# Kernel optimization log

Measured on AMD Instinct MI355X. Metric: run time of the kernel, lower is better.

Reference implementation:

```python
import jax, jax.numpy as jnp
import numpy as np

N_BOTTLENECK = 256  # must be a power of two for the butterfly network


def butterfly_ortho(x, theta, first_output_entry_positive=False):
    """FFT-like butterfly of Givens rotations over the last dim (size n, power of 2).
    Stage s pairs indices (i, i + 2^s); each pair gets one rotation angle.
    theta has (n/2)*log2(n) entries, consumed stage by stage.
    """
    n = x.shape[-1]
    stages = int(np.log2(n))
    idx = 0
    for s in range(stages):
        stride = 1 << s
        nb = n // (2 * stride)
        th = theta[idx: idx + n // 2].reshape(nb, stride)
        idx += n // 2
        xr = x.reshape(-1, nb, 2, stride)  # [B, blocks, half, offset]
        a, b = xr[:, :, 0, :], xr[:, :, 1, :]
        c, sn = jnp.cos(th), jnp.sin(th)
        a2 = c * a - sn * b
        b2 = sn * a + c * b
        x = jnp.stack([a2, b2], axis=2).reshape(-1, n)
    if first_output_entry_positive:
        # convention flag: force sign of first output entry non-negative
        x = x.at[:, 0].set(jnp.abs(x[:, 0]))
    return x


def setup_inputs() -> dict:
    key = jax.random.key(0)
    ks = jax.random.split(key, 12)
    dims = [4096, 1024, 256, 1024, 4096]
    B = 16384

    def w(k, i, o):
        return (jax.random.normal(k, (i, o), dtype=jnp.float32) * (1.0 / np.sqrt(i)))

    inp = {
        "x": jax.random.normal(ks[0], (B, dims[0]), dtype=jnp.float32),
        "enc_w0": w(ks[1], dims[0], dims[1]),
        "enc_b0": jnp.zeros((dims[1],), jnp.float32),
        "enc_w1": w(ks[2], dims[1], dims[2]),
        "enc_b1": jnp.zeros((dims[2],), jnp.float32),
        "theta": jax.random.normal(ks[3], ((dims[2] // 2) * int(np.log2(dims[2])),), dtype=jnp.float32),
        "dec_w0": w(ks[4], dims[2], dims[3]),
        "dec_b0": jnp.zeros((dims[3],), jnp.float32),
        "out_w": w(ks[5], dims[3], dims[4]),
        "out_b": jnp.zeros((dims[4],), jnp.float32),
    }
    return inp


def reference(x, enc_w0, enc_b0, enc_w1, enc_b1, theta, dec_w0, dec_b0, out_w, out_b):
    # encoder: Linear + ReLU stack
    h = jax.nn.relu(x @ enc_w0 + enc_b0)
    h = jax.nn.relu(h @ enc_w1 + enc_b1)
    # orthogonal butterfly network at the bottleneck
    h = butterfly_ortho(h, theta, first_output_entry_positive=False)
    # decoder: Linear + ReLU stack, then plain Linear output layer
    h = jax.nn.relu(h @ dec_w0 + dec_b0)
    out = h @ out_w + out_b
    return out
```

## Files before the change

kernel.cpp:

```cpp
#include <hip/hip_runtime.h>

typedef __attribute__((ext_vector_type(8))) short short8v;
typedef __attribute__((ext_vector_type(4))) float f32x4;
typedef __attribute__((ext_vector_type(4))) unsigned int uint4v;
typedef __attribute__((ext_vector_type(4))) float float4v;

__device__ __forceinline__ unsigned short f2bf(float f) {
  union { float f; unsigned u; } v; v.f = f;
  unsigned r = v.u + 0x7fffu + ((v.u >> 16) & 1u);
  return (unsigned short)(r >> 16);
}
__device__ __forceinline__ float bf2f(unsigned short h) {
  union { unsigned u; float f; } v; v.u = ((unsigned)h) << 16;
  return v.f;
}
__device__ __forceinline__ unsigned pack2(float a, float b) {
  return (unsigned)f2bf(a) | ((unsigned)f2bf(b) << 16);
}

__device__ __forceinline__ void gload_lds16(const void* g, void* l) {
  __builtin_amdgcn_global_load_lds(
      (const __attribute__((address_space(1))) void*)g,
      (__attribute__((address_space(3))) void*)l, 16, 0, 0);
}

#define SBAR() __builtin_amdgcn_s_barrier()
#define SCHED0() __builtin_amdgcn_sched_barrier(0)
#define LGKM(n) do { asm volatile("s_waitcnt lgkmcnt(" #n ")" ::: "memory"); \
                     __builtin_amdgcn_sched_barrier(0); } while (0)
#define VMW(n) asm volatile("s_waitcnt vmcnt(" #n ")" ::: "memory")

__global__ void f32_to_bf16(const float* __restrict__ in, unsigned short* __restrict__ out,
                            size_t n8) {
  size_t i = (size_t)blockIdx.x * blockDim.x + threadIdx.x;
  const size_t stride = (size_t)gridDim.x * blockDim.x;
  for (; i < n8; i += stride) {
    const float4v* p = (const float4v*)(in + i * 8);
    float4v a = __builtin_nontemporal_load(p);
    float4v b = __builtin_nontemporal_load(p + 1);
    uint4v r;
    r.x = pack2(a.x, a.y); r.y = pack2(a.z, a.w);
    r.z = pack2(b.x, b.y); r.w = pack2(b.z, b.w);
    *(uint4v*)(out + i * 8) = r;
  }
}

__global__ void transpose_bf16(const float* __restrict__ W, unsigned short* __restrict__ WT,
                               int K, int N) {
  __shared__ float t[32][33];
  const int kb = blockIdx.x * 32, nb = blockIdx.y * 32;
  const int tx = threadIdx.x, ty = threadIdx.y;
  #pragma unroll
  for (int y = 0; y < 4; ++y)
    t[ty + y*8][tx] = W[(size_t)(kb + ty + y*8) * N + nb + tx];
  __syncthreads();
  #pragma unroll
  for (int y = 0; y < 4; ++y) {
    const int n = nb + ty + y*8;
    WT[(size_t)n * K + kb + tx] = f2bf(t[tx][ty + y*8]);
  }
}

__global__ void trig_kernel(const float* __restrict__ theta, float* __restrict__ ct,
                            float* __restrict__ st, int n) {
  const int i = blockIdx.x * 256 + threadIdx.x;
  if (i < n) {
    float s, c;
    sincosf(theta[i], &s, &c);
    ct[i] = c; st[i] = s;
  }
}

__global__ void butterfly_kernel(const unsigned short* __restrict__ X,
                                 unsigned short* __restrict__ Y,
                                 const float* __restrict__ ct, const float* __restrict__ st) {
  __shared__ float L[2][256];
  const int tid = threadIdx.x;
  const size_t base = (size_t)blockIdx.x * 512;
  const unsigned v = *(const unsigned*)(X + base + tid * 2);
  const int r = tid >> 7;
  const int col = (tid * 2) & 255;
  L[r][col]     = bf2f((unsigned short)(v & 0xffffu));
  L[r][col + 1] = bf2f((unsigned short)(v >> 16));
  __syncthreads();
  const int p = tid & 127;
  #pragma unroll
  for (int s = 0; s < 8; ++s) {
    const int stride = 1 << s;
    const int t = p & (stride - 1);
    const int i = ((p >> s) << (s + 1)) + t;
    const int j = i + stride;
    const float c  = ct[s * 128 + p];
    const float sn = st[s * 128 + p];
    const float a = L[r][i], b = L[r][j];
    L[r][i] = c * a - sn * b;
    L[r][j] = sn * a + c * b;
    __syncthreads();
  }
  const unsigned lo = f2bf(L[r][col]);
  const unsigned hi = f2bf(L[r][col + 1]);
  *(unsigned*)(Y + base + tid * 2) = lo | (hi << 16);
}

template<bool RELU, bool OUT_F32>
__global__ __launch_bounds__(256) void gemm_kernel(
    const unsigned short* __restrict__ A, const unsigned short* __restrict__ BT,
    const float* __restrict__ bias, void* __restrict__ Cp,
    int M, int N, int K)
{
  __shared__ __align__(16) unsigned short As[128 * 32];
  __shared__ __align__(16) unsigned short Bs[128 * 32];
  const int tid = threadIdx.x;
  const int lane = tid & 63;
  const int w = tid >> 6;
  const int wm = w >> 1, wn = w & 1;
  const int n0 = blockIdx.x * 128;
  const int m0 = blockIdx.y * 128;
  const int g4 = lane >> 4;
  const int ml = lane & 15;

  f32x4 acc[4][4];
  #pragma unroll
  for (int i = 0; i < 4; ++i)
    #pragma unroll
    for (int n = 0; n < 4; ++n)
      #pragma unroll
      for (int e = 0; e < 4; ++e)
        acc[i][n][e] = 0.0f;

  const int nkt = K >> 5;
  const int srow = w * 32 + (lane >> 2);
  const int scol = (lane & 3) * 8;

  for (int kt = 0; kt < nkt; ++kt) {
    const int k0 = kt << 5;
    #pragma unroll
    for (int q = 0; q < 2; ++q) {
      const unsigned short* gb = BT + (size_t)(n0 + srow + q * 16) * K + k0 + scol;
      gload_lds16(gb, Bs + w * 1024 + q * 512);
      const unsigned short* ga = A + (size_t)(m0 + srow + q * 16) * K + k0 + scol;
      gload_lds16(ga, As + w * 1024 + q * 512);
    }
    __syncthreads();
    short8v af[4], bf[4];
    #pragma unroll
    for (int i = 0; i < 4; ++i)
      af[i] = *(const short8v*)(As + (wm * 64 + i * 16 + ml) * 32 + g4 * 8);
    #pragma unroll
    for (int n = 0; n < 4; ++n)
      bf[n] = *(const short8v*)(Bs + (wn * 64 + n * 16 + ml) * 32 + g4 * 8);
    #pragma unroll
    for (int i = 0; i < 4; ++i)
      #pragma unroll
      for (int n = 0; n < 4; ++n)
        acc[i][n] = __builtin_amdgcn_mfma_f32_16x16x32_bf16(af[i], bf[n], acc[i][n], 0, 0, 0);
    __syncthreads();
  }
  #pragma unroll
  for (int n = 0; n < 4; ++n) {
    const int col = n0 + wn * 64 + n * 16 + ml;
    const float bv = bias[col];
    #pragma unroll
    for (int i = 0; i < 4; ++i) {
      const int rowb = m0 + wm * 64 + i * 16 + g4 * 4;
      #pragma unroll
      for (int r = 0; r < 4; ++r) {
        float v = acc[i][n][r] + bv;
        if constexpr (RELU) v = fmaxf(v, 0.0f);
        if constexpr (OUT_F32)
          __builtin_nontemporal_store(v, &((float*)Cp)[(size_t)(rowb + r) * N + col]);
        else
          ((unsigned short*)Cp)[(size_t)(rowb + r) * N + col] = f2bf(v);
      }
    }
  }
}

template<int MI0, int NI0>
__device__ __forceinline__ void mfma8(f32x4 (&acc)[8][4], const short8v (&a)[4],
                                      const short8v (&b)[2]) {
  __builtin_amdgcn_s_setprio(1);
  #pragma unroll
  for (int mi = 0; mi < 4; ++mi)
    #pragma unroll
    for (int ni = 0; ni < 2; ++ni)
      acc[MI0+mi][NI0+ni] = __builtin_amdgcn_mfma_f32_16x16x32_bf16(
          a[mi], b[ni], acc[MI0+mi][NI0+ni], 0, 0, 0);
  __builtin_amdgcn_s_setprio(0);
}

template<bool RELU, bool OUT_F32>
__global__ __launch_bounds__(512) void gemm256(
    const unsigned short* __restrict__ A, const unsigned short* __restrict__ BT,
    const float* __restrict__ bias, void* __restrict__ Cp,
    int M, int N, int K)
{
  __shared__ __align__(16) unsigned char lds[131072];
  const int tid = threadIdx.x;
  const int lane = tid & 63, w = tid >> 6;
  const int wm = w >> 2, wn = w & 3;
  const int ml = lane & 15, g4 = lane >> 4;

  const int nx = gridDim.x;
  const int nwg = nx * (int)gridDim.y;
  const int bid = blockIdx.y * nx + blockIdx.x;
  const int cpx = nwg >> 3;
  const int swz = (bid & 7) * cpx + (bid >> 3);
  const int n0 = (swz % nx) * 256;
  const int m0 = (swz / nx) * 256;

  const int rloc = w * 8 + (lane >> 3);
  const int scol = ((lane & 7) ^ (lane >> 3)) * 8;
  const int ldst = w * 1024;

  const int off0 = (g4 * 16) ^ ((ml & 7) << 4);
  const int aoff = (wm * 128 + ml) * 128 + off0;
  const int boff = (wn * 64 + ml) * 128 + off0;

  const int NT = K >> 6;
  const int NJ = NT >> 1;

  f32x4 acc[8][4];
  #pragma unroll
  for (int mi = 0; mi < 8; ++mi)
    #pragma unroll
    for (int ni = 0; ni < 4; ++ni)
      #pragma unroll
      for (int e = 0; e < 4; ++e)
        acc[mi][ni][e] = 0.0f;

  auto stA = [&](int d, int h, int t) {
    const unsigned short* g0 = A + (size_t)(m0 + h * 128 + rloc) * K + t * 64 + scol;
    unsigned char* l0 = lds + d * 65536 + h * 16384 + ldst;
    gload_lds16(g0, l0);
    gload_lds16(g0 + (size_t)64 * K, l0 + 8192);
  };
  auto stB = [&](int d, int h, int t) {
    const unsigned short* g0 = BT + (size_t)(n0 + h * 128 + rloc) * K + t * 64 + scol;
    unsigned char* l0 = lds + d * 65536 + 32768 + h * 16384 + ldst;
    gload_lds16(g0, l0);
    gload_lds16(g0 + (size_t)64 * K, l0 + 8192);
  };
  auto rdA0 = [&](short8v (&dst)[4], int d, int mh) {
    #pragma unroll
    for (int mi = 0; mi < 4; ++mi)
      dst[mi] = *(const short8v*)(lds + d * 65536 + aoff + (mh * 4 + mi) * 2048);
  };
  auto rdA1 = [&](short8v (&dst)[4], int d, int mh) {
    #pragma unroll
    for (int mi = 0; mi < 4; ++mi)
      dst[mi] = *(const short8v*)(lds + ((d * 65536 + aoff + (mh * 4 + mi) * 2048) ^ 64));
  };
  auto rdB0 = [&](short8v (&dst)[2], int d, int nh) {
    #pragma unroll
    for (int ni = 0; ni < 2; ++ni)
      dst[ni] = *(const short8v*)(lds + d * 65536 + 32768 + boff + (nh * 2 + ni) * 2048);
  };
  auto rdB1 = [&](short8v (&dst)[2], int d, int nh) {
    #pragma unroll
    for (int ni = 0; ni < 2; ++ni)
      dst[ni] = *(const short8v*)(lds + ((d * 65536 + 32768 + boff + (nh * 2 + ni) * 2048) ^ 64));
  };

  short8v aR_0[4], aR_1[4], aS_0[4], aS_1[4];
  short8v bR0_0[2], bR0_1[2], bR1_0[2], bR1_1[2];

  stB(0, 0, 0); stB(0, 1, 0); stA(0, 0, 0); stA(0, 1, 0);
  stB(1, 0, 1); stB(1, 1, 1);
  VMW(4);
  SBAR();

  for (int j = 0; j < NJ; ++j) {
    const int t1 = 2 * j + 1;
    const int t2 = (2 * j + 2 < NT) ? 2 * j + 2 : NT - 1;
    const int t3 = (2 * j + 3 < NT) ? 2 * j + 3 : NT - 1;

    rdB0(bR0_0, 0, 0); rdA0(aR_0, 0, 0);
    SCHED0();
    rdB1(bR0_1, 0, 0); rdA1(aR_1, 0, 0);
    stA(1, 0, t1);
    SBAR(); LGKM(6);
    mfma8<0, 0>(acc, aR_0, bR0_0);
    LGKM(0);
    mfma8<0, 0>(acc, aR_1, bR0_1);
    SBAR();
    rdB0(bR1_0, 0, 1);
    SCHED0();
    rdB1(bR1_1, 0, 1);
    stA(1, 1, t1);
    SBAR(); LGKM(2);
    mfma8<0, 2>(acc, aR_0, bR1_0);
    LGKM(0);
    mfma8<0, 2>(acc, aR_1, bR1_1);
    SBAR();
    rdA0(aS_0, 0, 1);
    SCHED0();
    rdA1(aS_1, 0, 1);
    stB(0, 0, t2);
    SBAR(); LGKM(4);
    mfma8<4, 0>(acc, aS_0, bR0_0);
    LGKM(0);
    mfma8<4, 0>(acc, aS_1, bR0_1);
    SBAR();
    stB(0, 1, t2);
    SBAR();
    mfma8<4, 2>(acc, aS_0, bR1_0);
    mfma8<4, 2>(acc, aS_1, bR1_1);
    VMW(4);
    SBAR();

    rdB0(bR0_0, 1, 0); rdA0(aR_0, 1, 0);
    SCHED0();
    rdB1(bR0_1, 1, 0); rdA1(aR_1, 1, 0);
    stA(0, 0, t2);
    SBAR(); LGKM(6);
    mfma8<0, 0>(acc, aR_0, bR0_0);
    LGKM(0);
    mfma8<0, 0>(acc, aR_1, bR0_1);
    SBAR();
    rdB0(bR1_0, 1, 1);
    SCHED0();
    rdB1(bR1_1, 1, 1);
    stA(0, 1, t2);
    SBAR(); LGKM(2);
    mfma8<0, 2>(acc, aR_0, bR1_0);
    LGKM(0);
    mfma8<0, 2>(acc, aR_1, bR1_1);
    SBAR();
    rdA0(aS_0, 1, 1);
    SCHED0();
    rdA1(aS_1, 1, 1);
    stB(1, 0, t3);
    SBAR(); LGKM(4);
    mfma8<4, 0>(acc, aS_0, bR0_0);
    LGKM(0);
    mfma8<4, 0>(acc, aS_1, bR0_1);
    SBAR();
    stB(1, 1, t3);
    SBAR();
    mfma8<4, 2>(acc, aS_0, bR1_0);
    mfma8<4, 2>(acc, aS_1, bR1_1);
    VMW(4);
    SBAR();
  }

  #pragma unroll
  for (int ni = 0; ni < 4; ++ni) {
    const int col = n0 + wn * 64 + ni * 16 + ml;
    const float bv = bias[col];
    #pragma unroll
    for (int mi = 0; mi < 8; ++mi) {
      const int rowb = m0 + wm * 128 + mi * 16 + g4 * 4;
      #pragma unroll
      for (int r = 0; r < 4; ++r) {
        float v = acc[mi][ni][r] + bv;
        if constexpr (RELU) v = fmaxf(v, 0.0f);
        if constexpr (OUT_F32)
          __builtin_nontemporal_store(v, &((float*)Cp)[(size_t)(rowb + r) * N + col]);
        else
          ((unsigned short*)Cp)[(size_t)(rowb + r) * N + col] = f2bf(v);
      }
    }
  }
}

extern "C" void kernel_launch(void* const* d_in, const int* in_sizes, int n_in,
                              void* d_out, int out_size, void* d_ws, size_t ws_size,
                              hipStream_t stream) {
  const float* x      = (const float*)d_in[0];
  const float* enc_w0 = (const float*)d_in[1];
  const float* enc_b0 = (const float*)d_in[2];
  const float* enc_w1 = (const float*)d_in[3];
  const float* enc_b1 = (const float*)d_in[4];
  const float* theta  = (const float*)d_in[5];
  const float* dec_w0 = (const float*)d_in[6];
  const float* dec_b0 = (const float*)d_in[7];
  const float* out_w  = (const float*)d_in[8];
  const float* out_b  = (const float*)d_in[9];
  float* out = (float*)d_out;

  char* ws = (char*)d_ws;
  unsigned short* xb  = (unsigned short*)(ws);
  unsigned short* wt0 = (unsigned short*)(ws + 134217728);
  unsigned short* wt1 = (unsigned short*)(ws + 142606336);
  unsigned short* wt2 = (unsigned short*)(ws + 143130624);
  unsigned short* wt3 = (unsigned short*)(ws + 143654912);
  unsigned short* h1  = (unsigned short*)(ws + 152043520);
  unsigned short* h2  = (unsigned short*)(ws + 185597952);
  unsigned short* h2b = (unsigned short*)(ws + 193986560);
  unsigned short* h3  = h1;
  float* ct = (float*)(ws + 202375168);
  float* st = ct + 1024;

  const int B = 16384;

  f32_to_bf16<<<2048, 256, 0, stream>>>(x, xb, (size_t)B * 4096 / 8);
  transpose_bf16<<<dim3(4096/32, 1024/32), dim3(32, 8), 0, stream>>>(enc_w0, wt0, 4096, 1024);
  transpose_bf16<<<dim3(1024/32,  256/32), dim3(32, 8), 0, stream>>>(enc_w1, wt1, 1024, 256);
  transpose_bf16<<<dim3( 256/32, 1024/32), dim3(32, 8), 0, stream>>>(dec_w0, wt2, 256, 1024);
  transpose_bf16<<<dim3(1024/32, 4096/32), dim3(32, 8), 0, stream>>>(out_w,  wt3, 1024, 4096);
  trig_kernel<<<4, 256, 0, stream>>>(theta, ct, st, 1024);

  gemm256<true,  false><<<dim3(1024/256, B/256), 512, 0, stream>>>(xb, wt0, enc_b0, h1, B, 1024, 4096);
  gemm_kernel<true,  false><<<dim3( 256/128, B/128), 256, 0, stream>>>(h1, wt1, enc_b1, h2, B, 256, 1024);
  butterfly_kernel<<<B/2, 256, 0, stream>>>(h2, h2b, ct, st);
  gemm_kernel<true,  false><<<dim3(1024/128, B/128), 256, 0, stream>>>(h2b, wt2, dec_b0, h3, B, 1024, 256);
  gemm256<false, true ><<<dim3(4096/256, B/256), 512, 0, stream>>>(h3, wt3, out_b, out, B, 4096, 1024);
}
```

Measured before the change: 394.6 us.

## Fuse fp32-to-bf16 input conversion into first encoder GEMM A-tile loads

Removes the standalone f32_to_bf16 pass over x. The first gemm256 now loads fp32 A tiles into registers, packs them to bf16 and writes them to LDS inside the pipelined loop, instead of using direct global-to-LDS loads. This saves a full write and re-read of the 128 MB bf16 copy of x. In exchange the GEMM reads twice as many A bytes from global memory, holds more registers, and adds VALU pack work plus extra LDS stores and waits in the main loop. Each output tile column block also re-reads the fp32 A rows.

```diff
diff --git a/kernel.cpp b/kernel.cpp
--- a/kernel.cpp
+++ b/kernel.cpp
@@ -29,21 +29,6 @@
 #define LGKM(n) do { asm volatile("s_waitcnt lgkmcnt(" #n ")" ::: "memory"); \
                      __builtin_amdgcn_sched_barrier(0); } while (0)
 #define VMW(n) asm volatile("s_waitcnt vmcnt(" #n ")" ::: "memory")
-
-__global__ void f32_to_bf16(const float* __restrict__ in, unsigned short* __restrict__ out,
-                            size_t n8) {
-  size_t i = (size_t)blockIdx.x * blockDim.x + threadIdx.x;
-  const size_t stride = (size_t)gridDim.x * blockDim.x;
-  for (; i < n8; i += stride) {
-    const float4v* p = (const float4v*)(in + i * 8);
-    float4v a = __builtin_nontemporal_load(p);
-    float4v b = __builtin_nontemporal_load(p + 1);
-    uint4v r;
-    r.x = pack2(a.x, a.y); r.y = pack2(a.z, a.w);
-    r.z = pack2(b.x, b.y); r.w = pack2(b.z, b.w);
-    *(uint4v*)(out + i * 8) = r;
-  }
-}
 
 __global__ void transpose_bf16(const float* __restrict__ W, unsigned short* __restrict__ WT,
                                int K, int N) {
@@ -189,9 +174,9 @@
   __builtin_amdgcn_s_setprio(0);
 }
 
-template<bool RELU, bool OUT_F32>
+template<bool A_F32, bool RELU, bool OUT_F32>
 __global__ __launch_bounds__(512) void gemm256(
-    const unsigned short* __restrict__ A, const unsigned short* __restrict__ BT,
+    const void* __restrict__ Ap, const unsigned short* __restrict__ BT,
     const float* __restrict__ bias, void* __restrict__ Cp,
     int M, int N, int K)
 {
@@ -220,6 +205,9 @@
   const int NT = K >> 6;
   const int NJ = NT >> 1;
 
+  const unsigned short* Ab = (const unsigned short*)Ap;
+  const float* Af = (const float*)Ap;
+
   f32x4 acc[8][4];
   #pragma unroll
   for (int mi = 0; mi < 8; ++mi)
@@ -230,7 +218,7 @@
         acc[mi][ni][e] = 0.0f;
 
   auto stA = [&](int d, int h, int t) {
-    const unsigned short* g0 = A + (size_t)(m0 + h * 128 + rloc) * K + t * 64 + scol;
+    const unsigned short* g0 = Ab + (size_t)(m0 + h * 128 + rloc) * K + t * 64 + scol;
     unsigned char* l0 = lds + d * 65536 + h * 16384 + ldst;
     gload_lds16(g0, l0);
     gload_lds16(g0 + (size_t)64 * K, l0 + 8192);
@@ -241,6 +229,29 @@
     gload_lds16(g0, l0);
     gload_lds16(g0 + (size_t)64 * K, l0 + 8192);
   };
+
+  float4v av[8];
+  auto ldA = [&](int h, int t) {
+    const float* g = Af + (size_t)(m0 + h * 128 + rloc) * K + t * 64 + scol;
+    av[h*4+0] = __builtin_nontemporal_load((const float4v*)g);
+    av[h*4+1] = __builtin_nontemporal_load((const float4v*)(g + 4));
+    av[h*4+2] = __builtin_nontemporal_load((const float4v*)(g + (size_t)64 * K));
+    av[h*4+3] = __builtin_nontemporal_load((const float4v*)(g + (size_t)64 * K + 4));
+  };
+  auto pwA = [&](int d) {
+    #pragma unroll
+    for (int h = 0; h < 2; ++h) {
+      uint4v w0, w1;
+      w0.x = pack2(av[h*4+0].x, av[h*4+0].y); w0.y = pack2(av[h*4+0].z, av[h*4+0].w);
+      w0.z = pack2(av[h*4+1].x, av[h*4+1].y); w0.w = pack2(av[h*4+1].z, av[h*4+1].w);
+      w1.x = pack2(av[h*4+2].x, av[h*4+2].y); w1.y = pack2(av[h*4+2].z, av[h*4+2].w);
+      w1.z = pack2(av[h*4+3].x, av[h*4+3].y); w1.w = pack2(av[h*4+3].z, av[h*4+3].w);
+      unsigned char* l0 = lds + d * 65536 + h * 16384 + ldst + lane * 16;
+      *(uint4v*)l0 = w0;
+      *(uint4v*)(l0 + 8192) = w1;
+    }
+  };
+
   auto rdA0 = [&](short8v (&dst)[4], int d, int mh) {
     #pragma unroll
     for (int mi = 0; mi < 4; ++mi)
@@ -265,10 +276,21 @@
   short8v aR_0[4], aR_1[4], aS_0[4], aS_1[4];
   short8v bR0_0[2], bR0_1[2], bR1_0[2], bR1_1[2];
 
-  stB(0, 0, 0); stB(0, 1, 0); stA(0, 0, 0); stA(0, 1, 0);
-  stB(1, 0, 1); stB(1, 1, 1);
-  VMW(4);
-  SBAR();
+  if constexpr (A_F32) {
+    stB(0, 0, 0); stB(0, 1, 0);
+    ldA(0, 0); ldA(1, 0); SCHED0();
+    stB(1, 0, 1); stB(1, 1, 1);
+    VMW(4);
+    SCHED0();
+    pwA(0);
+    LGKM(0);
+    SBAR();
+  } else {
+    stB(0, 0, 0); stB(0, 1, 0); stA(0, 0, 0); stA(0, 1, 0);
+    stB(1, 0, 1); stB(1, 1, 1);
+    VMW(4);
+    SBAR();
+  }
 
   for (int j = 0; j < NJ; ++j) {
     const int t1 = 2 * j + 1;
@@ -278,7 +300,7 @@
     rdB0(bR0_0, 0, 0); rdA0(aR_0, 0, 0);
     SCHED0();
     rdB1(bR0_1, 0, 0); rdA1(aR_1, 0, 0);
-    stA(1, 0, t1);
+    if constexpr (A_F32) { ldA(0, t1); SCHED0(); } else { stA(1, 0, t1); }
     SBAR(); LGKM(6);
     mfma8<0, 0>(acc, aR_0, bR0_0);
     LGKM(0);
@@ -287,7 +309,7 @@
     rdB0(bR1_0, 0, 1);
     SCHED0();
     rdB1(bR1_1, 0, 1);
-    stA(1, 1, t1);
+    if constexpr (A_F32) { ldA(1, t1); SCHED0(); } else { stA(1, 1, t1); }
     SBAR(); LGKM(2);
     mfma8<0, 2>(acc, aR_0, bR1_0);
     LGKM(0);
@@ -302,17 +324,29 @@
     LGKM(0);
     mfma8<4, 0>(acc, aS_1, bR0_1);
     SBAR();
-    stB(0, 1, t2);
-    SBAR();
-    mfma8<4, 2>(acc, aS_0, bR1_0);
-    mfma8<4, 2>(acc, aS_1, bR1_1);
-    VMW(4);
-    SBAR();
+    if constexpr (A_F32) {
+      VMW(2);
+      SCHED0();
+      pwA(1);
+      stB(0, 1, t2);
+      LGKM(0);
+      SBAR();
+      mfma8<4, 2>(acc, aS_0, bR1_0);
+      mfma8<4, 2>(acc, aS_1, bR1_1);
+      SBAR();
+    } else {
+      stB(0, 1, t2);
+      SBAR();
+      mfma8<4, 2>(acc, aS_0, bR1_0);
+      mfma8<4, 2>(acc, aS_1, bR1_1);
+      VMW(4);
+      SBAR();
+    }
 
     rdB0(bR0_0, 1, 0); rdA0(aR_0, 1, 0);
     SCHED0();
     rdB1(bR0_1, 1, 0); rdA1(aR_1, 1, 0);
-    stA(0, 0, t2);
+    if constexpr (A_F32) { ldA(0, t2); SCHED0(); } else { stA(0, 0, t2); }
     SBAR(); LGKM(6);
     mfma8<0, 0>(acc, aR_0, bR0_0);
     LGKM(0);
@@ -321,7 +355,7 @@
     rdB0(bR1_0, 1, 1);
     SCHED0();
     rdB1(bR1_1, 1, 1);
-    stA(0, 1, t2);
+    if constexpr (A_F32) { ldA(1, t2); SCHED0(); } else { stA(0, 1, t2); }
     SBAR(); LGKM(2);
     mfma8<0, 2>(acc, aR_0, bR1_0);
     LGKM(0);
@@ -336,12 +370,24 @@
     LGKM(0);
     mfma8<4, 0>(acc, aS_1, bR0_1);
     SBAR();
-    stB(1, 1, t3);
-    SBAR();
-    mfma8<4, 2>(acc, aS_0, bR1_0);
-    mfma8<4, 2>(acc, aS_1, bR1_1);
-    VMW(4);
-    SBAR();
+    if constexpr (A_F32) {
+      VMW(2);
+      SCHED0();
+      pwA(0);
+      stB(1, 1, t3);
+      LGKM(0);
+      SBAR();
+      mfma8<4, 2>(acc, aS_0, bR1_0);
+      mfma8<4, 2>(acc, aS_1, bR1_1);
+      SBAR();
+    } else {
+      stB(1, 1, t3);
+      SBAR();
+      mfma8<4, 2>(acc, aS_0, bR1_0);
+      mfma8<4, 2>(acc, aS_1, bR1_1);
+      VMW(4);
+      SBAR();
+    }
   }
 
   #pragma unroll
@@ -380,7 +426,6 @@
   float* out = (float*)d_out;
 
   char* ws = (char*)d_ws;
-  unsigned short* xb  = (unsigned short*)(ws);
   unsigned short* wt0 = (unsigned short*)(ws + 134217728);
   unsigned short* wt1 = (unsigned short*)(ws + 142606336);
   unsigned short* wt2 = (unsigned short*)(ws + 143130624);
@@ -394,16 +439,15 @@
 
   const int B = 16384;
 
-  f32_to_bf16<<<2048, 256, 0, stream>>>(x, xb, (size_t)B * 4096 / 8);
   transpose_bf16<<<dim3(4096/32, 1024/32), dim3(32, 8), 0, stream>>>(enc_w0, wt0, 4096, 1024);
   transpose_bf16<<<dim3(1024/32,  256/32), dim3(32, 8), 0, stream>>>(enc_w1, wt1, 1024, 256);
   transpose_bf16<<<dim3( 256/32, 1024/32), dim3(32, 8), 0, stream>>>(dec_w0, wt2, 256, 1024);
   transpose_bf16<<<dim3(1024/32, 4096/32), dim3(32, 8), 0, stream>>>(out_w,  wt3, 1024, 4096);
   trig_kernel<<<4, 256, 0, stream>>>(theta, ct, st, 1024);
 
-  gemm256<true,  false><<<dim3(1024/256, B/256), 512, 0, stream>>>(xb, wt0, enc_b0, h1, B, 1024, 4096);
+  gemm256<true,  true,  false><<<dim3(1024/256, B/256), 512, 0, stream>>>(x, wt0, enc_b0, h1, B, 1024, 4096);
   gemm_kernel<true,  false><<<dim3( 256/128, B/128), 256, 0, stream>>>(h1, wt1, enc_b1, h2, B, 256, 1024);
   butterfly_kernel<<<B/2, 256, 0, stream>>>(h2, h2b, ct, st);
   gemm_kernel<true,  false><<<dim3(1024/128, B/128), 256, 0, stream>>>(h2b, wt2, dec_b0, h3, B, 1024, 256);
-  gemm256<false, true ><<<dim3(4096/256, B/256), 512, 0, stream>>>(h3, wt3, out_b, out, B, 4096, 1024);
-}
+  gemm256<false, false, true ><<<dim3(4096/256, B/256), 512, 0, stream>>>(h3, wt3, out_b, out, B, 4096, 1024);
+}
```

Measured after the change: 515.7 us. 30.7% more time.
